# Optimization experiments

Measured on AMD Instinct MI355X. Metric: run time of the kernel, lower is better.

Reference implementation:

```python
import jax, jax.numpy as jnp
import numpy as np

EMBED = 512
HEADS = 8
DH = EMBED // HEADS  # 64
M = 256              # num_landmarks
ITERS = 6            # pinv iterations
SCALE = DH ** -0.5
RES_K = 33           # lucidrains residual_conv_kernel default


def _layer_norm(x, g, b, eps=1e-5):
    mu = jnp.mean(x, axis=-1, keepdims=True)
    var = jnp.mean((x - mu) ** 2, axis=-1, keepdims=True)
    return (x - mu) / jnp.sqrt(var + eps) * g + b


def _pinv_iter(x, iters=ITERS):
    # Moore-Penrose iterative pseudo-inverse (lucidrains nystrom-attention)
    abs_x = jnp.abs(x)
    denom = jnp.max(abs_x.sum(-1)) * jnp.max(abs_x.sum(-2))
    z = jnp.swapaxes(x, -1, -2) / denom
    I = jnp.eye(x.shape[-1], dtype=x.dtype)
    for _ in range(iters):
        xz = x @ z
        z = 0.25 * z @ (13 * I - xz @ (15 * I - xz @ (7 * I - xz)))
    return z


def _dwconv2d(x, w, b):
    # x: [B,C,H,W], w: [C,1,kh,kw] depthwise, SAME padding (odd kernels == k//2)
    out = jax.lax.conv_general_dilated(x, w, (1, 1), 'SAME',
                                       dimension_numbers=('NCHW', 'OIHW', 'NCHW'),
                                       feature_group_count=x.shape[1])
    return out + b[None, :, None, None]


def _nystrom_attn(x, Wqkv, Wo, bo, res_w):
    # x: [B, n, EMBED]; pad at FRONT so n divisible by M (matches F.pad(..., padding, 0) semantics)
    b, n, _ = x.shape
    pad = (M - n % M) % M
    x = jnp.pad(x, ((0, 0), (pad, 0), (0, 0)))
    npad = n + pad
    qkv = x @ Wqkv.T                               # [b, npad, 3*EMBED]
    q, k, v = jnp.split(qkv, 3, axis=-1)
    to_heads = lambda t: t.reshape(b, npad, HEADS, DH).transpose(0, 2, 1, 3)  # bhnd
    q, k, v = to_heads(q), to_heads(k), to_heads(v)
    q = q * SCALE
    l = npad // M
    q_land = q.reshape(b, HEADS, M, l, DH).mean(3)  # [b,h,M,d]
    k_land = k.reshape(b, HEADS, M, l, DH).mean(3)
    s1 = jnp.einsum('bhnd,bhmd->bhnm', q, k_land)
    s2 = jnp.einsum('bhmd,bhld->bhml', q_land, k_land)
    s3 = jnp.einsum('bhmd,bhnd->bhmn', q_land, k)
    a1 = jax.nn.softmax(s1, -1)
    a2 = jax.nn.softmax(s2, -1)
    a3 = jax.nn.softmax(s3, -1)
    a2_inv = _pinv_iter(a2)
    out = a1 @ (a2_inv @ (a3 @ v))                 # [b,h,npad,d]
    # residual depthwise conv over v: channels=heads, spatial=(npad, DH), kernel (33,1)
    res = jax.lax.conv_general_dilated(v, res_w, (1, 1), 'SAME',
                                       dimension_numbers=('NCHW', 'OIHW', 'NCHW'),
                                       feature_group_count=HEADS)
    out = out + res
    out = out.transpose(0, 2, 1, 3).reshape(b, npad, EMBED)
    out = out @ Wo.T + bo
    return out[:, -n:]                             # drop front padding


def setup_inputs() -> dict:
    key = jax.random.key(0)
    ks = jax.random.split(key, 32)
    s = 0.02
    inp = {}
    inp['data'] = jax.random.normal(ks[0], (4, 4096, 1536), jnp.float32)
    inp['W1'] = jax.random.normal(ks[1], (EMBED, 1536), jnp.float32) * s
    inp['b1'] = jnp.zeros((EMBED,), jnp.float32)
    inp['cls_token'] = jax.random.normal(ks[2], (1, 1, EMBED), jnp.float32)
    for li, base in ((1, 3), (2, 9)):
        inp[f'ln{li}_g'] = jnp.ones((EMBED,), jnp.float32)
        inp[f'ln{li}_b'] = jnp.zeros((EMBED,), jnp.float32)
        inp[f'Wqkv{li}'] = jax.random.normal(ks[base], (3 * EMBED, EMBED), jnp.float32) * s
        inp[f'Wo{li}'] = jax.random.normal(ks[base + 1], (EMBED, EMBED), jnp.float32) * s
        inp[f'bo{li}'] = jnp.zeros((EMBED,), jnp.float32)
        inp[f'res{li}'] = jax.random.normal(ks[base + 2], (HEADS, 1, RES_K, 1), jnp.float32) * s
    inp['pw7'] = jax.random.normal(ks[15], (EMBED, 1, 7, 7), jnp.float32) * s
    inp['pb7'] = jnp.zeros((EMBED,), jnp.float32)
    inp['pw5'] = jax.random.normal(ks[16], (EMBED, 1, 5, 5), jnp.float32) * s
    inp['pb5'] = jnp.zeros((EMBED,), jnp.float32)
    inp['pw3'] = jax.random.normal(ks[17], (EMBED, 1, 3, 3), jnp.float32) * s
    inp['pb3'] = jnp.zeros((EMBED,), jnp.float32)
    inp['lnf_g'] = jnp.ones((EMBED,), jnp.float32)
    inp['lnf_b'] = jnp.zeros((EMBED,), jnp.float32)
    inp['W2'] = jax.random.normal(ks[18], (2, EMBED), jnp.float32) * s
    inp['b2'] = jnp.zeros((2,), jnp.float32)
    return inp


def reference(data, W1, b1, cls_token, ln1_g, ln1_b, Wqkv1, Wo1, bo1, res1,
              ln2_g, ln2_b, Wqkv2, Wo2, bo2, res2,
              pw7, pb7, pw5, pb5, pw3, pb3, lnf_g, lnf_b, W2, b2):
    h = jax.nn.relu(data @ W1.T + b1)              # [B, N, EMBED]
    B, N, C = h.shape
    grid = int(np.ceil(np.sqrt(N)))
    add = grid * grid - N
    if add > 0:
        h = jnp.concatenate([h, h[:, :add]], axis=1)
    cls = jnp.broadcast_to(cls_token, (B, 1, C))
    h = jnp.concatenate([cls, h], axis=1)          # [B, 1+grid^2, C]
    # TransLayer 1
    h = h + _nystrom_attn(_layer_norm(h, ln1_g, ln1_b), Wqkv1, Wo1, bo1, res1)
    # PPEG
    cls_t, feat = h[:, :1], h[:, 1:]
    cnn = feat.transpose(0, 2, 1).reshape(B, C, grid, grid)
    x = _dwconv2d(cnn, pw7, pb7) + cnn + _dwconv2d(cnn, pw5, pb5) + _dwconv2d(cnn, pw3, pb3)
    feat = x.reshape(B, C, grid * grid).transpose(0, 2, 1)
    h = jnp.concatenate([cls_t, feat], axis=1)
    # TransLayer 2
    h = h + _nystrom_attn(_layer_norm(h, ln2_g, ln2_b), Wqkv2, Wo2, bo2, res2)
    h = _layer_norm(h, lnf_g, lnf_b)
    cls_feat = h[:, 0]
    logits = cls_feat @ W2.T + b2
    Y_prob = jax.nn.softmax(logits, -1)
    Y_hat = jnp.argmax(Y_prob, -1)
    return logits, Y_prob, Y_hat
```

## Files before the change

kernel.cpp:

```cpp
#include <hip/hip_runtime.h>
#include <math.h>

#define EMBED 512
#define HEADS 8
#define DH 64
#define MM 256
#define LSEG 17
#define NPAD 4352
#define NTOK 4097
#define N0 4096
#define BATCH 4
#define CIN 1536
#define QSCALE 0.125f
#define BH 32
#define NSEG 17

typedef float fp32x4 __attribute__((ext_vector_type(4)));
typedef short bf16x8 __attribute__((ext_vector_type(8)));
typedef short bf16x4 __attribute__((ext_vector_type(4)));
typedef unsigned short u16;

__device__ __forceinline__ unsigned short f2bf(float f) {
  unsigned int u = __float_as_uint(f);
  u += 0x7fffu + ((u >> 16) & 1u);
  return (unsigned short)(u >> 16);
}
__device__ __forceinline__ float bf2f(unsigned short u) {
  return __uint_as_float((unsigned)u << 16);
}

__device__ __forceinline__ float block_sum(float v, float* red) {
  #pragma unroll
  for (int o = 1; o < 64; o <<= 1) v += __shfl_xor(v, o);
  int lane = threadIdx.x & 63, wid = threadIdx.x >> 6;
  if (lane == 0) red[wid] = v;
  __syncthreads();
  float r = red[0] + red[1] + red[2] + red[3];
  __syncthreads();
  return r;
}
__device__ __forceinline__ float block_max(float v, float* red) {
  #pragma unroll
  for (int o = 1; o < 64; o <<= 1) v = fmaxf(v, __shfl_xor(v, o));
  int lane = threadIdx.x & 63, wid = threadIdx.x >> 6;
  if (lane == 0) red[wid] = v;
  __syncthreads();
  float r = fmaxf(fmaxf(red[0], red[1]), fmaxf(red[2], red[3]));
  __syncthreads();
  return r;
}

__global__ void f2bf_kernel(const float* __restrict__ in, u16* __restrict__ out, int n) {
  int t = (blockIdx.x * 256 + threadIdx.x) * 8;
  if (t >= n) return;
  float4 a = *(const float4*)&in[t];
  float4 b = *(const float4*)&in[t + 4];
  bf16x8 pk;
  pk[0]=(short)f2bf(a.x); pk[1]=(short)f2bf(a.y); pk[2]=(short)f2bf(a.z); pk[3]=(short)f2bf(a.w);
  pk[4]=(short)f2bf(b.x); pk[5]=(short)f2bf(b.y); pk[6]=(short)f2bf(b.z); pk[7]=(short)f2bf(b.w);
  *(bf16x8*)&out[t] = pk;
}

__global__ __launch_bounds__(256) void gemm_abt(
    const u16* __restrict__ A, const u16* __restrict__ W,
    int Mrows, int Ncols, int K, const float* __restrict__ bias,
    float* __restrict__ fout, float* __restrict__ fout2,
    u16* __restrict__ uo0, u16* __restrict__ uo1, u16* __restrict__ uo2,
    int mode)
{
  __shared__ u16 As[64][40];
  __shared__ u16 Ws[128][40];
  int tid = threadIdx.x;
  int lane = tid & 63;
  int wv = tid >> 6;
  int rowBase = blockIdx.y * 64, colBase = blockIdx.x * 128;
  int quad = lane >> 4;
  int l15 = lane & 15;
  int sr = tid >> 2;
  int skc = (tid & 3) * 8;

  fp32x4 acc[8];
  #pragma unroll
  for (int i = 0; i < 8; i++) acc[i] = fp32x4{0,0,0,0};

  for (int kb = 0; kb < K; kb += 32) {
    __syncthreads();
    {
      int grow = rowBase + sr;
      bf16x8 av;
      if (grow < Mrows) av = *(const bf16x8*)&A[(size_t)grow * K + kb + skc];
      else { bf16x8 z = {0,0,0,0,0,0,0,0}; av = z; }
      *(bf16x8*)&As[sr][skc] = av;
    }
    #pragma unroll
    for (int h = 0; h < 2; h++) {
      int r = sr + h * 64;
      *(bf16x8*)&Ws[r][skc] =
          *(const bf16x8*)&W[(size_t)(colBase + r) * K + kb + skc];
    }
    __syncthreads();
    bf16x8 aF = *(const bf16x8*)&As[wv * 16 + l15][quad * 8];
    #pragma unroll
    for (int ct = 0; ct < 8; ct++) {
      bf16x8 bF = *(const bf16x8*)&Ws[ct * 16 + l15][quad * 8];
      acc[ct] = __builtin_amdgcn_mfma_f32_16x16x32_bf16(aF, bF, acc[ct], 0, 0, 0);
    }
  }

  #pragma unroll
  for (int ct = 0; ct < 8; ct++) {
    int col = colBase + ct * 16 + l15;
    #pragma unroll
    for (int i = 0; i < 4; i++) {
      int row = rowBase + wv * 16 + quad * 4 + i;
      if (row >= Mrows) continue;
      float v = acc[ct][i];
      if (mode == 0) {
        v += bias[col];
        v = fmaxf(v, 0.f);
        int b = row / N0, n = row % N0;
        fout[((size_t)b * NTOK + 1 + n) * EMBED + col] = v;
      } else if (mode == 1) {
        int b = row / NPAD, n = row % NPAD;
        int sec = col / EMBED;
        int hh = (col % EMBED) / DH;
        int d = col & 63;
        u16* dst = (sec == 0) ? uo0 : ((sec == 1) ? uo1 : uo2);
        if (sec == 0) v *= QSCALE;
        dst[(((size_t)b * HEADS + hh) * NPAD + n) * DH + d] = f2bf(v);
      } else if (mode == 2) {
        v += bias[col];
        fout[(size_t)row * EMBED + col] += v;
      } else {
        v += bias[col];
        float full = fout[(size_t)row * EMBED + col] + v;
        fout[(size_t)row * EMBED + col] = full;
        int b = row / NTOK, t = row % NTOK;
        if (t > 0) fout2[((size_t)b * N0 + (t - 1)) * EMBED + col] = full;
      }
    }
  }
}

__global__ __launch_bounds__(256) void gemm_nn2(
    const u16* __restrict__ A, const u16* __restrict__ Bc,
    u16* __restrict__ Cr, u16* __restrict__ Cc,
    int Nsize, float beta, float sgn, float gamma)
{
  __shared__ u16 As[64][40];
  __shared__ u16 Bs[64][40];
  int batch = blockIdx.z;
  const u16* Ab = A + (size_t)batch * MM * MM;
  const u16* Bb = Bc + (size_t)batch * MM * Nsize;
  int tid = threadIdx.x;
  int lane = tid & 63, wv = tid >> 6, quad = lane >> 4, l15 = lane & 15;
  int rowBase = blockIdx.y * 64, colBase = blockIdx.x * 64;
  int sr = tid >> 2, skc = (tid & 3) * 8;
  fp32x4 acc[4] = {fp32x4{0,0,0,0}, fp32x4{0,0,0,0}, fp32x4{0,0,0,0}, fp32x4{0,0,0,0}};

  for (int kb = 0; kb < MM; kb += 32) {
    __syncthreads();
    *(bf16x8*)&As[sr][skc] = *(const bf16x8*)&Ab[(size_t)(rowBase + sr) * MM + kb + skc];
    *(bf16x8*)&Bs[sr][skc] = *(const bf16x8*)&Bb[(size_t)(colBase + sr) * MM + kb + skc];
    __syncthreads();
    bf16x8 aF = *(const bf16x8*)&As[wv * 16 + l15][quad * 8];
    #pragma unroll
    for (int ct = 0; ct < 4; ct++) {
      bf16x8 bF = *(const bf16x8*)&Bs[ct * 16 + l15][quad * 8];
      acc[ct] = __builtin_amdgcn_mfma_f32_16x16x32_bf16(aF, bF, acc[ct], 0, 0, 0);
    }
  }

  #pragma unroll
  for (int ct = 0; ct < 4; ct++) {
    int col = colBase + ct * 16 + l15;
    #pragma unroll
    for (int i = 0; i < 4; i++) {
      int row = rowBase + wv * 16 + quad * 4 + i;
      float v = sgn * acc[ct][i];
      if (beta != 0.f) v += beta * bf2f(Ab[(size_t)row * MM + col]);
      v *= gamma;
      u16 o = f2bf(v);
      if (Cr) Cr[(size_t)batch * MM * Nsize + (size_t)row * Nsize + col] = o;
      if (Cc) Cc[(size_t)batch * MM * Nsize + (size_t)col * MM + row] = o;
    }
  }
}

__global__ void cls_kernel(const float* __restrict__ cls, float* __restrict__ h) {
  int t = blockIdx.x * blockDim.x + threadIdx.x;
  if (t >= BATCH * EMBED) return;
  int b = t / EMBED, c = t % EMBED;
  h[(size_t)b * NTOK * EMBED + c] = cls[c];
}

__global__ void zero_pad_kernel(u16* __restrict__ xpad) {
  int t = blockIdx.x * blockDim.x + threadIdx.x;
  const int per = 255 * EMBED;
  if (t >= BATCH * per) return;
  int b = t / per, r = t % per;
  xpad[(size_t)b * NPAD * EMBED + r] = 0;
}

__global__ __launch_bounds__(256) void ln_pad_kernel(
    const float* __restrict__ h, const float* __restrict__ g,
    const float* __restrict__ be, u16* __restrict__ xpad)
{
  __shared__ float red[4];
  int row = blockIdx.x;
  int b = row / NTOK, j = row % NTOK;
  const float* x = h + (size_t)row * EMBED;
  int tid = threadIdx.x;
  float v0 = x[tid], v1 = x[tid + 256];
  float mu = block_sum(v0 + v1, red) * (1.f / 512.f);
  float d0 = v0 - mu, d1 = v1 - mu;
  float var = block_sum(d0 * d0 + d1 * d1, red) * (1.f / 512.f);
  float inv = 1.f / sqrtf(var + 1e-5f);
  u16* o = xpad + ((size_t)b * NPAD + 255 + j) * EMBED;
  o[tid]       = f2bf(d0 * inv * g[tid]       + be[tid]);
  o[tid + 256] = f2bf(d1 * inv * g[tid + 256] + be[tid + 256]);
}

__global__ __launch_bounds__(256) void landmarks_kernel(
    const u16* __restrict__ q, const u16* __restrict__ k,
    float* __restrict__ qland, float* __restrict__ kland, u16* __restrict__ klandB)
{
  int bh = blockIdx.y;
  int m = blockIdx.x * 4 + (threadIdx.x >> 6);
  int d = threadIdx.x & 63;
  const u16* qb = q + (size_t)bh * NPAD * DH;
  const u16* kb = k + (size_t)bh * NPAD * DH;
  float sq = 0.f, sk = 0.f;
  int base = m * LSEG;
  #pragma unroll
  for (int t = 0; t < LSEG; t++) {
    sq += bf2f(qb[(size_t)(base + t) * DH + d]);
    sk += bf2f(kb[(size_t)(base + t) * DH + d]);
  }
  float kv = sk * (1.f / LSEG);
  qland[((size_t)bh * MM + m) * DH + d] = sq * (1.f / LSEG);
  kland[((size_t)bh * MM + m) * DH + d] = kv;
  klandB[((size_t)bh * MM + m) * DH + d] = f2bf(kv);
}

__global__ __launch_bounds__(256) void s2_softmax_kernel(
    const float* __restrict__ qland, const float* __restrict__ kland,
    u16* __restrict__ a2)
{
  __shared__ float qrow[64];
  __shared__ float red[4];
  int bh = blockIdx.y, m = blockIdx.x, tid = threadIdx.x;
  if (tid < 64) qrow[tid] = qland[((size_t)bh * MM + m) * DH + tid];
  __syncthreads();
  const float* kb = kland + (size_t)bh * MM * DH + (size_t)tid * DH;
  float s = 0.f;
  #pragma unroll 16
  for (int d = 0; d < 64; d++) s += qrow[d] * kb[d];
  float mx = block_max(s, red);
  float e = __expf(s - mx);
  float tot = block_sum(e, red);
  a2[((size_t)bh * MM + m) * MM + tid] = f2bf(e / tot);
}

__global__ void init_denom_kernel(float* __restrict__ denoms) {
  if (threadIdx.x < 2) denoms[threadIdx.x] = 0.f;
}

__global__ __launch_bounds__(256) void denom_kernel(
    const u16* __restrict__ a2, float* __restrict__ denoms)
{
  __shared__ float red[4];
  int bh = blockIdx.x, tid = threadIdx.x;
  const u16* A = a2 + (size_t)bh * MM * MM;
  float rs = 0.f, cs = 0.f;
  for (int j = 0; j < MM; j++) rs += bf2f(A[(size_t)tid * MM + j]);
  for (int i = 0; i < MM; i++) cs += bf2f(A[(size_t)i * MM + tid]);
  float mr = block_max(rs, red);
  float mc = block_max(cs, red);
  if (tid == 0) {
    atomicMax((int*)&denoms[0], __float_as_int(mr));
    atomicMax((int*)&denoms[1], __float_as_int(mc));
  }
}

__global__ __launch_bounds__(256) void z0_trans_kernel(
    const u16* __restrict__ a2, const float* __restrict__ denoms,
    u16* __restrict__ zr, u16* __restrict__ zc)
{
  __shared__ u16 tile[64][72];
  int bh = blockIdx.z, i0 = blockIdx.y * 64, j0 = blockIdx.x * 64;
  int tid = threadIdx.x;
  float inv = 1.f / (denoms[0] * denoms[1]);
  const u16* Ab = a2 + (size_t)bh * MM * MM;
  #pragma unroll
  for (int it = 0; it < 4; it++) {
    int idx = it * 1024 + tid * 4;
    int r = idx >> 6, c = idx & 63;
    bf16x4 v = *(const bf16x4*)&Ab[(size_t)(i0 + r) * MM + j0 + c];
    u16 o[4];
    #pragma unroll
    for (int j = 0; j < 4; j++) o[j] = f2bf(bf2f((unsigned short)v[j]) * inv);
    *(bf16x4*)&zc[(size_t)bh * MM * MM + (size_t)(i0 + r) * MM + j0 + c] = *(bf16x4*)o;
    #pragma unroll
    for (int j = 0; j < 4; j++) tile[c + j][r] = o[j];
  }
  __syncthreads();
  #pragma unroll
  for (int it = 0; it < 4; it++) {
    int idx = it * 1024 + tid * 4;
    int r = idx >> 6, c = idx & 63;
    u16 o[4] = {tile[r][c], tile[r][c + 1], tile[r][c + 2], tile[r][c + 3]};
    *(bf16x4*)&zr[(size_t)bh * MM * MM + (size_t)(j0 + r) * MM + i0 + c] = *(bf16x4*)o;
  }
}

__global__ __launch_bounds__(256) void a3v_part_mfma(
    const float* __restrict__ qland, const u16* __restrict__ k,
    const u16* __restrict__ v, u16* __restrict__ Opart,
    float* __restrict__ mpart, float* __restrict__ lpart)
{
  __shared__ __align__(16) u16 qs[64][40];
  __shared__ __align__(16) u16 ks[256][72];
  __shared__ __align__(16) u16 vt[64][72];
  int tid = threadIdx.x;
  int lane = tid & 63, wv = tid >> 6, quad = lane >> 4, l15 = lane & 15;
  int bh = blockIdx.y;
  int ltile = blockIdx.x & 3;
  int seg = blockIdx.x >> 2;
  int l0 = ltile * 64;
  int key0 = seg * 256;
  const float* qb = qland + (size_t)bh * MM * DH;
  const u16* kb = k + (size_t)bh * NPAD * DH;
  const u16* vb = v + (size_t)bh * NPAD * DH;

  {
    int sr = tid >> 2, dc = (tid & 3) * 16;
    const float4* p = (const float4*)&qb[(size_t)(l0 + sr) * DH + dc];
    float4 v0 = p[0], v1 = p[1], v2 = p[2], v3 = p[3];
    float va[16] = {v0.x,v0.y,v0.z,v0.w, v1.x,v1.y,v1.z,v1.w,
                    v2.x,v2.y,v2.z,v2.w, v3.x,v3.y,v3.z,v3.w};
    bf16x8 p0, p1;
    #pragma unroll
    for (int j = 0; j < 8; j++) { p0[j] = (short)f2bf(va[j]); p1[j] = (short)f2bf(va[8 + j]); }
    *(bf16x8*)&qs[sr][dc] = p0;
    *(bf16x8*)&qs[sr][dc + 8] = p1;
  }
  #pragma unroll
  for (int i = 0; i < 16; i++) {
    int idx = i * 1024 + tid * 4;
    int r = idx >> 6, c = idx & 63;
    *(bf16x4*)&ks[r][c] = *(const bf16x4*)&kb[(size_t)(key0 + r) * DH + c];
  }
  __syncthreads();

  fp32x4 sacc[16];
  #pragma unroll
  for (int ct = 0; ct < 16; ct++) sacc[ct] = fp32x4{0,0,0,0};
  bf16x8 aF0 = *(const bf16x8*)&qs[wv * 16 + l15][quad * 8];
  bf16x8 aF1 = *(const bf16x8*)&qs[wv * 16 + l15][32 + quad * 8];
  #pragma unroll
  for (int ct = 0; ct < 16; ct++) {
    bf16x8 b0 = *(const bf16x8*)&ks[ct * 16 + l15][quad * 8];
    bf16x8 b1 = *(const bf16x8*)&ks[ct * 16 + l15][32 + quad * 8];
    sacc[ct] = __builtin_amdgcn_mfma_f32_16x16x32_bf16(aF0, b0, sacc[ct], 0, 0, 0);
    sacc[ct] = __builtin_amdgcn_mfma_f32_16x16x32_bf16(aF1, b1, sacc[ct], 0, 0, 0);
  }

  float mrow[4], lrow[4];
  #pragma unroll
  for (int i = 0; i < 4; i++) {
    float m = -3.0e38f;
    #pragma unroll
    for (int ct = 0; ct < 16; ct++) m = fmaxf(m, sacc[ct][i]);
    #pragma unroll
    for (int o = 1; o < 16; o <<= 1) m = fmaxf(m, __shfl_xor(m, o));
    float s = 0.f;
    #pragma unroll
    for (int ct = 0; ct < 16; ct++) {
      float e = __expf(sacc[ct][i] - m);
      sacc[ct][i] = e;
      s += e;
    }
    #pragma unroll
    for (int o = 1; o < 16; o <<= 1) s += __shfl_xor(s, o);
    mrow[i] = m;
    lrow[i] = s;
  }
  __syncthreads();
  u16* P = &ks[0][0];
  #pragma unroll
  for (int ct = 0; ct < 16; ct++)
    #pragma unroll
    for (int i = 0; i < 4; i++)
      P[(size_t)(wv * 16 + quad * 4 + i) * 264 + ct * 16 + l15] = f2bf(sacc[ct][i]);
  __syncthreads();

  fp32x4 oacc[4] = {fp32x4{0,0,0,0}, fp32x4{0,0,0,0}, fp32x4{0,0,0,0}, fp32x4{0,0,0,0}};
  int dh = tid & 63, kgrp = tid >> 6;
  for (int ch = 0; ch < 4; ch++) {
    if (ch) __syncthreads();
    {
      int kbase = kgrp * 16;
      #pragma unroll
      for (int g = 0; g < 4; g++) {
        u16 pk[4];
        #pragma unroll
        for (int r = 0; r < 4; r++)
          pk[r] = vb[(size_t)(key0 + ch * 64 + kbase + g * 4 + r) * DH + dh];
        *(bf16x4*)&vt[dh][kbase + g * 4] = *(bf16x4*)pk;
      }
    }
    __syncthreads();
    #pragma unroll
    for (int ks2 = 0; ks2 < 2; ks2++) {
      bf16x8 aP = *(const bf16x8*)&P[(size_t)(wv * 16 + l15) * 264 + ch * 64 + ks2 * 32 + quad * 8];
      #pragma unroll
      for (int ct = 0; ct < 4; ct++) {
        bf16x8 bV = *(const bf16x8*)&vt[ct * 16 + l15][ks2 * 32 + quad * 8];
        oacc[ct] = __builtin_amdgcn_mfma_f32_16x16x32_bf16(aP, bV, oacc[ct], 0, 0, 0);
      }
    }
  }

  size_t base = ((size_t)seg * BH + bh) * MM + l0;
  #pragma unroll
  for (int ct = 0; ct < 4; ct++)
    #pragma unroll
    for (int i = 0; i < 4; i++) {
      int row = wv * 16 + quad * 4 + i;
      Opart[(base + row) * DH + ct * 16 + l15] = f2bf(oacc[ct][i]);
    }
  if (l15 == 0) {
    #pragma unroll
    for (int i = 0; i < 4; i++) {
      int row = wv * 16 + quad * 4 + i;
      mpart[base + row] = mrow[i];
      lpart[base + row] = lrow[i];
    }
  }
}

__global__ __launch_bounds__(256) void a3v_merge_kernel(
    const u16* __restrict__ Opart, const float* __restrict__ mpart,
    const float* __restrict__ lpart, u16* __restrict__ kvT)
{
  int bh = blockIdx.y;
  int lbase = blockIdx.x * 64;
  int d = threadIdx.x & 63, lsub = threadIdx.x >> 6;
  for (int li = lsub; li < 64; li += 4) {
    int lm = lbase + li;
    float M = -3.0e38f;
    #pragma unroll
    for (int s = 0; s < NSEG; s++)
      M = fmaxf(M, mpart[((size_t)s * BH + bh) * MM + lm]);
    float L = 0.f, O = 0.f;
    #pragma unroll
    for (int s = 0; s < NSEG; s++) {
      size_t idx = ((size_t)s * BH + bh) * MM + lm;
      float w = __expf(mpart[idx] - M);
      L += lpart[idx] * w;
      O += bf2f(Opart[idx * DH + d]) * w;
    }
    kvT[((size_t)bh * DH + d) * MM + lm] = f2bf(O / L);
  }
}

__global__ void prep_toep_kernel(const float* __restrict__ resw0,
                                 const float* __restrict__ resw1,
                                 u16* __restrict__ toepB)
{
  int i = blockIdx.x * 256 + threadIdx.x;
  if (i >= 2 * 8 * 64 * 96) return;
  int t = i % 96, r = (i / 96) % 64, hh = (i / (96 * 64)) % 8, l = i / (96 * 64 * 8);
  const float* rw = l ? resw1 : resw0;
  int tap = t - r;
  float v = (tap >= 0 && tap <= 32) ? rw[hh * 33 + tap] : 0.f;
  toepB[i] = f2bf(v);
}

__global__ __launch_bounds__(256, 4) void attn1_mfma(
    const u16* __restrict__ q, const u16* __restrict__ klandB,
    const u16* __restrict__ kv2T, const u16* __restrict__ v,
    const u16* __restrict__ toep, u16* __restrict__ attn)
{
  __shared__ __align__(16) u16 buf[64 * 264];
  int tid = threadIdx.x;
  int lane = tid & 63, wv = tid >> 6, quad = lane >> 4, l15 = lane & 15;
  int bh = blockIdx.y, b = bh >> 3, hh = bh & 7;
  int n0 = 255 + blockIdx.x * 64;
  const u16* qb  = q + (size_t)bh * NPAD * DH;
  const u16* klb = klandB + (size_t)bh * MM * DH;
  const u16* kvb = kv2T + (size_t)bh * DH * MM;
  const u16* vb  = v + (size_t)bh * NPAD * DH;
  const u16* tb  = toep + (size_t)hh * 64 * 96;

  int qrow = n0 + wv * 16 + l15; if (qrow > NPAD - 1) qrow = NPAD - 1;
  bf16x8 aF0 = *(const bf16x8*)&qb[(size_t)qrow * DH + quad * 8];
  bf16x8 aF1 = *(const bf16x8*)&qb[(size_t)qrow * DH + 32 + quad * 8];
  fp32x4 sacc[16];
  #pragma unroll
  for (int ct = 0; ct < 16; ct++) sacc[ct] = fp32x4{0,0,0,0};
  #pragma unroll
  for (int ct = 0; ct < 16; ct++) {
    bf16x8 b0 = *(const bf16x8*)&klb[(size_t)(ct * 16 + l15) * DH + quad * 8];
    bf16x8 b1 = *(const bf16x8*)&klb[(size_t)(ct * 16 + l15) * DH + 32 + quad * 8];
    sacc[ct] = __builtin_amdgcn_mfma_f32_16x16x32_bf16(aF0, b0, sacc[ct], 0, 0, 0);
    sacc[ct] = __builtin_amdgcn_mfma_f32_16x16x32_bf16(aF1, b1, sacc[ct], 0, 0, 0);
  }
  #pragma unroll
  for (int i = 0; i < 4; i++) {
    float m = -3.0e38f;
    #pragma unroll
    for (int ct = 0; ct < 16; ct++) m = fmaxf(m, sacc[ct][i]);
    #pragma unroll
    for (int o = 1; o < 16; o <<= 1) m = fmaxf(m, __shfl_xor(m, o));
    float s = 0.f;
    #pragma unroll
    for (int ct = 0; ct < 16; ct++) {
      float e = __expf(sacc[ct][i] - m);
      sacc[ct][i] = e;
      s += e;
    }
    #pragma unroll
    for (int o = 1; o < 16; o <<= 1) s += __shfl_xor(s, o);
    float inv = 1.f / s;
    #pragma unroll
    for (int ct = 0; ct < 16; ct++) sacc[ct][i] *= inv;
  }
  #pragma unroll
  for (int ct = 0; ct < 16; ct++)
    #pragma unroll
    for (int i = 0; i < 4; i++)
      buf[(size_t)(wv * 16 + quad * 4 + i) * 264 + ct * 16 + l15] = f2bf(sacc[ct][i]);
  __syncthreads();

  fp32x4 oacc[4] = {fp32x4{0,0,0,0}, fp32x4{0,0,0,0}, fp32x4{0,0,0,0}, fp32x4{0,0,0,0}};
  #pragma unroll
  for (int ks = 0; ks < 8; ks++) {
    bf16x8 aP = *(const bf16x8*)&buf[(size_t)(wv * 16 + l15) * 264 + ks * 32 + quad * 8];
    #pragma unroll
    for (int ct = 0; ct < 4; ct++) {
      bf16x8 bV = *(const bf16x8*)&kvb[(size_t)(ct * 16 + l15) * MM + ks * 32 + quad * 8];
      oacc[ct] = __builtin_amdgcn_mfma_f32_16x16x32_bf16(aP, bV, oacc[ct], 0, 0, 0);
    }
  }
  __syncthreads();

  {
    int d = lane;
    #pragma unroll
    for (int tt4 = 0; tt4 < 6; tt4++) {
      u16 vals[4];
      #pragma unroll
      for (int j = 0; j < 4; j++) {
        int t = wv * 24 + tt4 * 4 + j;
        int g = n0 - 16 + t;
        vals[j] = (g <= NPAD - 1) ? vb[(size_t)g * DH + d] : (u16)0;
      }
      *(bf16x4*)&buf[d * 104 + wv * 24 + tt4 * 4] = *(bf16x4*)vals;
    }
  }
  __syncthreads();

  #pragma unroll
  for (int kc = 0; kc < 3; kc++) {
    bf16x8 aT = *(const bf16x8*)&tb[(size_t)(wv * 16 + l15) * 96 + kc * 32 + quad * 8];
    #pragma unroll
    for (int ct = 0; ct < 4; ct++) {
      bf16x8 bW = *(const bf16x8*)&buf[(ct * 16 + l15) * 104 + kc * 32 + quad * 8];
      oacc[ct] = __builtin_amdgcn_mfma_f32_16x16x32_bf16(aT, bW, oacc[ct], 0, 0, 0);
    }
  }

  #pragma unroll
  for (int ct = 0; ct < 4; ct++) {
    int c = ct * 16 + l15;
    #pragma unroll
    for (int i = 0; i < 4; i++) {
      int rl = wv * 16 + quad * 4 + i;
      int n = n0 + rl;
      if (n > NPAD - 1) continue;
      attn[((size_t)b * NTOK + (n - 255)) * EMBED + hh * DH + c] = f2bf(oacc[ct][i]);
    }
  }
}

__global__ void prep_wcomb_kernel(
    const float* __restrict__ pw7, const float* __restrict__ pw5,
    const float* __restrict__ pw3, const float* __restrict__ pb7,
    const float* __restrict__ pb5, const float* __restrict__ pb3,
    float* __restrict__ wcomb, float* __restrict__ biasc)
{
  int i = blockIdx.x * blockDim.x + threadIdx.x;
  if (i < EMBED * 49) {
    int c = i / 49, tap = i % 49;
    int ky = tap / 7, kx = tap % 7;
    float v = pw7[c * 49 + tap];
    if (ky >= 1 && ky <= 5 && kx >= 1 && kx <= 5) v += pw5[c * 25 + (ky - 1) * 5 + (kx - 1)];
    if (ky >= 2 && ky <= 4 && kx >= 2 && kx <= 4) v += pw3[c * 9 + (ky - 2) * 3 + (kx - 2)];
    if (ky == 3 && kx == 3) v += 1.f;
    wcomb[tap * EMBED + c] = v;
  }
  if (i < EMBED) biasc[i] = pb7[i] + pb5[i] + pb3[i];
}

__global__ __launch_bounds__(256) void dwconv_kernel(
    const float* __restrict__ tmp, const float* __restrict__ wcomb,
    const float* __restrict__ biasc, float* __restrict__ h)
{
  __shared__ float4 wsm[49][32];
  int tx = threadIdx.x;
  int ty = threadIdx.y;
  int cb = blockIdx.x * 128;
  int c = cb + tx * 4;
  int b = blockIdx.z;
  int n = blockIdx.y * 8 + ty;
  int y = n >> 6, x = n & 63;
  int tid = ty * 32 + tx;
  for (int i = tid; i < 49 * 32; i += 256) {
    int tap = i >> 5, g = i & 31;
    wsm[tap][g] = *(const float4*)&wcomb[tap * EMBED + cb + g * 4];
  }
  __syncthreads();
  const float* src = tmp + (size_t)b * N0 * EMBED;
  float4 acc = *(const float4*)&biasc[c];
  #pragma unroll
  for (int ky = 0; ky < 7; ky++) {
    int yy = y + ky - 3;
    if (yy < 0 || yy >= 64) continue;
    #pragma unroll
    for (int kx = 0; kx < 7; kx++) {
      int xx = x + kx - 3;
      if (xx < 0 || xx >= 64) continue;
      float4 vv = *(const float4*)&src[((size_t)yy * 64 + xx) * EMBED + c];
      float4 w = wsm[ky * 7 + kx][tx];
      acc.x += vv.x * w.x;
      acc.y += vv.y * w.y;
      acc.z += vv.z * w.z;
      acc.w += vv.w * w.w;
    }
  }
  *(float4*)&h[((size_t)b * NTOK + 1 + n) * EMBED + c] = acc;
}

__global__ __launch_bounds__(256) void final_kernel(
    const float* __restrict__ h, const float* __restrict__ g,
    const float* __restrict__ be, const float* __restrict__ W2,
    const float* __restrict__ b2, float* __restrict__ out)
{
  __shared__ float red[4];
  int b = blockIdx.x, tid = threadIdx.x;
  const float* x = h + (size_t)b * NTOK * EMBED;
  float v0 = x[tid], v1 = x[tid + 256];
  float mu = block_sum(v0 + v1, red) * (1.f / 512.f);
  float d0 = v0 - mu, d1 = v1 - mu;
  float var = block_sum(d0 * d0 + d1 * d1, red) * (1.f / 512.f);
  float inv = 1.f / sqrtf(var + 1e-5f);
  float xn0 = d0 * inv * g[tid] + be[tid];
  float xn1 = d1 * inv * g[tid + 256] + be[tid + 256];
  float l0 = block_sum(xn0 * W2[tid] + xn1 * W2[tid + 256], red);
  float l1 = block_sum(xn0 * W2[512 + tid] + xn1 * W2[512 + tid + 256], red);
  if (tid == 0) {
    l0 += b2[0]; l1 += b2[1];
    out[b * 2 + 0] = l0;
    out[b * 2 + 1] = l1;
    float mx = fmaxf(l0, l1);
    float e0 = expf(l0 - mx), e1 = expf(l1 - mx);
    float s = e0 + e1;
    out[8 + b * 2 + 0] = e0 / s;
    out[8 + b * 2 + 1] = e1 / s;
    out[16 + b] = (l1 > l0) ? 1.f : 0.f;
  }
}

extern "C" void kernel_launch(void* const* d_in, const int* in_sizes, int n_in,
                              void* d_out, int out_size, void* d_ws, size_t ws_size,
                              hipStream_t stream)
{
  const float* data = (const float*)d_in[0];
  const float* W1   = (const float*)d_in[1];
  const float* b1   = (const float*)d_in[2];
  const float* cls  = (const float*)d_in[3];
  const float* lng[2]  = {(const float*)d_in[4],  (const float*)d_in[10]};
  const float* lnb[2]  = {(const float*)d_in[5],  (const float*)d_in[11]};
  const float* Wqkv[2] = {(const float*)d_in[6],  (const float*)d_in[12]};
  const float* Wo[2]   = {(const float*)d_in[7],  (const float*)d_in[13]};
  const float* bo[2]   = {(const float*)d_in[8],  (const float*)d_in[14]};
  const float* resw[2] = {(const float*)d_in[9],  (const float*)d_in[15]};
  const float* pw7 = (const float*)d_in[16];
  const float* pb7 = (const float*)d_in[17];
  const float* pw5 = (const float*)d_in[18];
  const float* pb5 = (const float*)d_in[19];
  const float* pw3 = (const float*)d_in[20];
  const float* pb3 = (const float*)d_in[21];
  const float* lnfg = (const float*)d_in[22];
  const float* lnfb = (const float*)d_in[23];
  const float* W2  = (const float*)d_in[24];
  const float* b2  = (const float*)d_in[25];

  float* ws = (float*)d_ws;
  size_t off = 0;
  auto alloc = [&](size_t n) { float* p = ws + off; off += n; return p; };
  float* hbuf   = alloc((size_t)BATCH * NTOK * EMBED);
  float* xpadf  = alloc((size_t)BATCH * NPAD * EMBED);
  float* qbuff  = alloc((size_t)BH * NPAD * DH);
  float* kbuff  = alloc((size_t)BH * NPAD * DH);
  float* vbuff  = alloc((size_t)BH * NPAD * DH);
  float* qland  = alloc((size_t)BH * MM * DH);
  float* kland  = alloc((size_t)BH * MM * DH);
  float* klandBf= alloc((size_t)BH * MM * DH / 2);
  float* a2f    = alloc((size_t)BH * MM * MM / 2);
  float* zaRf   = alloc((size_t)BH * MM * MM / 2);
  float* zaCf   = alloc((size_t)BH * MM * MM / 2);
  float* zbRf   = alloc((size_t)BH * MM * MM / 2);
  float* zbCf   = alloc((size_t)BH * MM * MM / 2);
  float* xzRf   = alloc((size_t)BH * MM * MM / 2);
  float* xzCf   = alloc((size_t)BH * MM * MM / 2);
  float* t1Cf   = alloc((size_t)BH * MM * MM / 2);
  float* t2Cf   = alloc((size_t)BH * MM * MM / 2);
  float* kvTf   = alloc((size_t)BH * MM * DH / 2);
  float* kv2Tf  = alloc((size_t)BH * MM * DH / 2);
  float* wqkvbf = alloc((size_t)2 * 3 * EMBED * EMBED / 2);
  float* wobf   = alloc((size_t)2 * EMBED * EMBED / 2);
  float* toepf  = alloc((size_t)2 * 8 * 64 * 96 / 2);
  float* wcomb  = alloc(49 * EMBED);
  float* biasc  = alloc(EMBED);
  float* denoms = alloc(64);
  float* mpart  = alloc((size_t)NSEG * BH * MM);
  float* lpart  = alloc((size_t)NSEG * BH * MM);

  u16* xpadB = (u16*)xpadf;
  u16* qB = (u16*)qbuff;
  u16* kB = (u16*)kbuff;
  u16* vB = (u16*)vbuff;
  u16* klandB = (u16*)klandBf;
  u16* a2B = (u16*)a2f;
  u16* zaR = (u16*)zaRf; u16* zaC = (u16*)zaCf;
  u16* zbR = (u16*)zbRf; u16* zbC = (u16*)zbCf;
  u16* xzR = (u16*)xzRf; u16* xzC = (u16*)xzCf;
  u16* t1C = (u16*)t1Cf; u16* t2C = (u16*)t2Cf;
  u16* kvT = (u16*)kvTf; u16* kv2T = (u16*)kv2Tf;
  u16* attnB = xpadB;
  u16* OpartB = zaR;
  u16* databf = (u16*)qbuff;
  u16* W1bf = (u16*)vbuff;
  u16* WqkvB[2] = {(u16*)wqkvbf, (u16*)wqkvbf + (size_t)3 * EMBED * EMBED};
  u16* WoB[2]   = {(u16*)wobf,   (u16*)wobf + (size_t)EMBED * EMBED};
  u16* toepB[2] = {(u16*)toepf,  (u16*)toepf + (size_t)8 * 64 * 96};
  float* convtmp = qbuff;

  int ndata = BATCH * N0 * CIN;
  f2bf_kernel<<<dim3((ndata / 8 + 255) / 256), 256, 0, stream>>>(data, databf, ndata);
  f2bf_kernel<<<dim3((EMBED * CIN / 8 + 255) / 256), 256, 0, stream>>>(W1, W1bf, EMBED * CIN);
  for (int l = 0; l < 2; l++) {
    f2bf_kernel<<<dim3((3 * EMBED * EMBED / 8 + 255) / 256), 256, 0, stream>>>(Wqkv[l], WqkvB[l], 3 * EMBED * EMBED);
    f2bf_kernel<<<dim3((EMBED * EMBED / 8 + 255) / 256), 256, 0, stream>>>(Wo[l], WoB[l], EMBED * EMBED);
  }
  prep_toep_kernel<<<dim3((2 * 8 * 64 * 96 + 255) / 256), 256, 0, stream>>>(
      resw[0], resw[1], (u16*)toepf);

  gemm_abt<<<dim3(EMBED / 128, (BATCH * N0) / 64), 256, 0, stream>>>(
      databf, W1bf, BATCH * N0, EMBED, CIN, b1, hbuf, nullptr, nullptr, nullptr, nullptr, 0);
  cls_kernel<<<dim3((BATCH * EMBED + 255) / 256), 256, 0, stream>>>(cls, hbuf);

  for (int layer = 0; layer < 2; layer++) {
    ln_pad_kernel<<<dim3(BATCH * NTOK), 256, 0, stream>>>(hbuf, lng[layer], lnb[layer], xpadB);
    zero_pad_kernel<<<dim3((BATCH * 255 * EMBED + 255) / 256), 256, 0, stream>>>(xpadB);
    gemm_abt<<<dim3((3 * EMBED) / 128, (BATCH * NPAD) / 64), 256, 0, stream>>>(
        xpadB, WqkvB[layer], BATCH * NPAD, 3 * EMBED, EMBED, nullptr,
        nullptr, nullptr, qB, kB, vB, 1);
    landmarks_kernel<<<dim3(MM / 4, BH), 256, 0, stream>>>(qB, kB, qland, kland, klandB);
    s2_softmax_kernel<<<dim3(MM, BH), 256, 0, stream>>>(qland, kland, a2B);
    init_denom_kernel<<<1, 64, 0, stream>>>(denoms);
    denom_kernel<<<dim3(BH), 256, 0, stream>>>(a2B, denoms);

    a3v_part_mfma<<<dim3(4 * NSEG, BH), 256, 0, stream>>>(
        qland, kB, vB, OpartB, mpart, lpart);
    a3v_merge_kernel<<<dim3(MM / 64, BH), 256, 0, stream>>>(OpartB, mpart, lpart, kvT);

    z0_trans_kernel<<<dim3(4, 4, BH), 256, 0, stream>>>(a2B, denoms, zaR, zaC);
    u16 *zinR = zaR, *zinC = zaC, *zoutR = zbR, *zoutC = zbC;
    for (int it = 0; it < 6; it++) {
      gemm_nn2<<<dim3(4, 4, BH), 256, 0, stream>>>(a2B, zinC, xzR, xzC, MM, 0.f, 1.f, 1.f);
      gemm_nn2<<<dim3(4, 4, BH), 256, 0, stream>>>(xzR, xzC, nullptr, t1C, MM, 7.f, -1.f, 1.f);
      gemm_nn2<<<dim3(4, 4, BH), 256, 0, stream>>>(xzR, t1C, nullptr, t2C, MM, 15.f, -1.f, 1.f);
      gemm_nn2<<<dim3(4, 4, BH), 256, 0, stream>>>(zinR, t2C, zoutR, zoutC, MM, 13.f, -1.f, 0.25f);
      u16* t;
      t = zinR; zinR = zoutR; zoutR = t;
      t = zinC; zinC = zoutC; zoutC = t;
    }
    gemm_nn2<<<dim3(1, 4, BH), 256, 0, stream>>>(zinR, kvT, nullptr, kv2T, DH, 0.f, 1.f, 1.f);
    attn1_mfma<<<dim3((NTOK + 63) / 64, BH), 256, 0, stream>>>(
        qB, klandB, kv2T, vB, toepB[layer], attnB);
    gemm_abt<<<dim3(EMBED / 128, (BATCH * NTOK + 63) / 64), 256, 0, stream>>>(
        attnB, WoB[layer], BATCH * NTOK, EMBED, EMBED, bo[layer], hbuf,
        (layer == 0) ? convtmp : nullptr, nullptr, nullptr, nullptr,
        (layer == 0) ? 3 : 2);

    if (layer == 0) {
      prep_wcomb_kernel<<<dim3((EMBED * 49 + 255) / 256), 256, 0, stream>>>(
          pw7, pw5, pw3, pb7, pb5, pb3, wcomb, biasc);
      dwconv_kernel<<<dim3(EMBED / 128, N0 / 8, BATCH), dim3(32, 8), 0, stream>>>(
          convtmp, wcomb, biasc, hbuf);
    }
  }

  final_kernel<<<dim3(BATCH), 256, 0, stream>>>(hbuf, lnfg, lnfb, W2, b2, (float*)d_out);
}
```

Baseline: 1.617 ms.

## Restructure pinv iteration into three GEMM stages and batch loads in attention kernel

The Newton-Schulz pseudo-inverse step is expanded algebraically as 0.25·(zY)(7Y−Y²) − 3.75·zY + 3.25·z. The two independent products, Y·(7I−Y) and z·Y, run in one merged launch, which cuts each iteration from four dependent GEMM launches to three. Separately, attn1_mfma now preloads groups of B-fragments into registers before issuing MFMAs, and its launch bounds drop from 4 to 2 blocks per CU. That trades occupancy for more in-flight loads. The reordered polynomial changes where bf16 rounding happens, so numerics shift slightly.

Measured after the change: 1.589 ms. No clear change (-1.7%).

```diff
diff --git a/kernel.cpp b/kernel.cpp
--- a/kernel.cpp
+++ b/kernel.cpp
@@ -142,10 +142,11 @@
   }
 }
 
-__global__ __launch_bounds__(256) void gemm_nn2(
+__global__ __launch_bounds__(256) void pinv_gemm(
     const u16* __restrict__ A, const u16* __restrict__ Bc,
+    const u16* __restrict__ E,
     u16* __restrict__ Cr, u16* __restrict__ Cc,
-    int Nsize, float beta, float sgn, float gamma)
+    int Nsize, float gamma, float beta, float eps)
 {
   __shared__ u16 As[64][40];
   __shared__ u16 Bs[64][40];
@@ -177,12 +178,57 @@
     #pragma unroll
     for (int i = 0; i < 4; i++) {
       int row = rowBase + wv * 16 + quad * 4 + i;
-      float v = sgn * acc[ct][i];
+      float v = gamma * acc[ct][i];
       if (beta != 0.f) v += beta * bf2f(Ab[(size_t)row * MM + col]);
-      v *= gamma;
+      if (eps != 0.f)  v += eps * bf2f(E[(size_t)batch * MM * MM + (size_t)row * MM + col]);
       u16 o = f2bf(v);
       if (Cr) Cr[(size_t)batch * MM * Nsize + (size_t)row * Nsize + col] = o;
       if (Cc) Cc[(size_t)batch * MM * Nsize + (size_t)col * MM + row] = o;
+    }
+  }
+}
+
+__global__ __launch_bounds__(256) void pinv_um(
+    const u16* __restrict__ YR, const u16* __restrict__ YC,
+    const u16* __restrict__ zR, u16* __restrict__ UC, u16* __restrict__ MR)
+{
+  __shared__ u16 As[64][40];
+  __shared__ u16 Bs[64][40];
+  int which = blockIdx.z >> 5;
+  int batch = blockIdx.z & 31;
+  const u16* Ab = (which ? zR : YR) + (size_t)batch * MM * MM;
+  const u16* Bb = YC + (size_t)batch * MM * MM;
+  int tid = threadIdx.x;
+  int lane = tid & 63, wv = tid >> 6, quad = lane >> 4, l15 = lane & 15;
+  int rowBase = blockIdx.y * 64, colBase = blockIdx.x * 64;
+  int sr = tid >> 2, skc = (tid & 3) * 8;
+  fp32x4 acc[4] = {fp32x4{0,0,0,0}, fp32x4{0,0,0,0}, fp32x4{0,0,0,0}, fp32x4{0,0,0,0}};
+
+  for (int kb = 0; kb < MM; kb += 32) {
+    __syncthreads();
+    *(bf16x8*)&As[sr][skc] = *(const bf16x8*)&Ab[(size_t)(rowBase + sr) * MM + kb + skc];
+    *(bf16x8*)&Bs[sr][skc] = *(const bf16x8*)&Bb[(size_t)(colBase + sr) * MM + kb + skc];
+    __syncthreads();
+    bf16x8 aF = *(const bf16x8*)&As[wv * 16 + l15][quad * 8];
+    #pragma unroll
+    for (int ct = 0; ct < 4; ct++) {
+      bf16x8 bF = *(const bf16x8*)&Bs[ct * 16 + l15][quad * 8];
+      acc[ct] = __builtin_amdgcn_mfma_f32_16x16x32_bf16(aF, bF, acc[ct], 0, 0, 0);
+    }
+  }
+
+  #pragma unroll
+  for (int ct = 0; ct < 4; ct++) {
+    int col = colBase + ct * 16 + l15;
+    #pragma unroll
+    for (int i = 0; i < 4; i++) {
+      int row = rowBase + wv * 16 + quad * 4 + i;
+      if (which == 0) {
+        float v = 7.f * bf2f(Ab[(size_t)row * MM + col]) - acc[ct][i];
+        UC[(size_t)batch * MM * MM + (size_t)col * MM + row] = f2bf(v);
+      } else {
+        MR[(size_t)batch * MM * MM + (size_t)row * MM + col] = f2bf(acc[ct][i]);
+      }
     }
   }
 }
@@ -478,7 +524,7 @@
   toepB[i] = f2bf(v);
 }
 
-__global__ __launch_bounds__(256, 4) void attn1_mfma(
+__global__ __launch_bounds__(256, 2) void attn1_mfma(
     const u16* __restrict__ q, const u16* __restrict__ klandB,
     const u16* __restrict__ kv2T, const u16* __restrict__ v,
     const u16* __restrict__ toep, u16* __restrict__ attn)
@@ -501,11 +547,20 @@
   #pragma unroll
   for (int ct = 0; ct < 16; ct++) sacc[ct] = fp32x4{0,0,0,0};
   #pragma unroll
-  for (int ct = 0; ct < 16; ct++) {
-    bf16x8 b0 = *(const bf16x8*)&klb[(size_t)(ct * 16 + l15) * DH + quad * 8];
-    bf16x8 b1 = *(const bf16x8*)&klb[(size_t)(ct * 16 + l15) * DH + 32 + quad * 8];
-    sacc[ct] = __builtin_amdgcn_mfma_f32_16x16x32_bf16(aF0, b0, sacc[ct], 0, 0, 0);
-    sacc[ct] = __builtin_amdgcn_mfma_f32_16x16x32_bf16(aF1, b1, sacc[ct], 0, 0, 0);
+  for (int g = 0; g < 2; g++) {
+    bf16x8 b0[8], b1[8];
+    #pragma unroll
+    for (int j = 0; j < 8; j++) {
+      int ct = g * 8 + j;
+      b0[j] = *(const bf16x8*)&klb[(size_t)(ct * 16 + l15) * DH + quad * 8];
+      b1[j] = *(const bf16x8*)&klb[(size_t)(ct * 16 + l15) * DH + 32 + quad * 8];
+    }
+    #pragma unroll
+    for (int j = 0; j < 8; j++) {
+      int ct = g * 8 + j;
+      sacc[ct] = __builtin_amdgcn_mfma_f32_16x16x32_bf16(aF0, b0[j], sacc[ct], 0, 0, 0);
+      sacc[ct] = __builtin_amdgcn_mfma_f32_16x16x32_bf16(aF1, b1[j], sacc[ct], 0, 0, 0);
+    }
   }
   #pragma unroll
   for (int i = 0; i < 4; i++) {
@@ -536,13 +591,21 @@
 
   fp32x4 oacc[4] = {fp32x4{0,0,0,0}, fp32x4{0,0,0,0}, fp32x4{0,0,0,0}, fp32x4{0,0,0,0}};
   #pragma unroll
-  for (int ks = 0; ks < 8; ks++) {
-    bf16x8 aP = *(const bf16x8*)&buf[(size_t)(wv * 16 + l15) * 264 + ks * 32 + quad * 8];
-    #pragma unroll
-    for (int ct = 0; ct < 4; ct++) {
-      bf16x8 bV = *(const bf16x8*)&kvb[(size_t)(ct * 16 + l15) * MM + ks * 32 + quad * 8];
-      oacc[ct] = __builtin_amdgcn_mfma_f32_16x16x32_bf16(aP, bV, oacc[ct], 0, 0, 0);
-    }
+  for (int g = 0; g < 2; g++) {
+    bf16x8 ap[4], bv[4][4];
+    #pragma unroll
+    for (int j = 0; j < 4; j++) {
+      int ks = g * 4 + j;
+      ap[j] = *(const bf16x8*)&buf[(size_t)(wv * 16 + l15) * 264 + ks * 32 + quad * 8];
+      #pragma unroll
+      for (int ct = 0; ct < 4; ct++)
+        bv[j][ct] = *(const bf16x8*)&kvb[(size_t)(ct * 16 + l15) * MM + ks * 32 + quad * 8];
+    }
+    #pragma unroll
+    for (int j = 0; j < 4; j++)
+      #pragma unroll
+      for (int ct = 0; ct < 4; ct++)
+        oacc[ct] = __builtin_amdgcn_mfma_f32_16x16x32_bf16(ap[j], bv[j][ct], oacc[ct], 0, 0, 0);
   }
   __syncthreads();
 
@@ -562,13 +625,18 @@
   }
   __syncthreads();
 
-  #pragma unroll
-  for (int kc = 0; kc < 3; kc++) {
-    bf16x8 aT = *(const bf16x8*)&tb[(size_t)(wv * 16 + l15) * 96 + kc * 32 + quad * 8];
-    #pragma unroll
-    for (int ct = 0; ct < 4; ct++) {
-      bf16x8 bW = *(const bf16x8*)&buf[(ct * 16 + l15) * 104 + kc * 32 + quad * 8];
-      oacc[ct] = __builtin_amdgcn_mfma_f32_16x16x32_bf16(aT, bW, oacc[ct], 0, 0, 0);
+  {
+    bf16x8 at[3];
+    #pragma unroll
+    for (int kc = 0; kc < 3; kc++)
+      at[kc] = *(const bf16x8*)&tb[(size_t)(wv * 16 + l15) * 96 + kc * 32 + quad * 8];
+    #pragma unroll
+    for (int kc = 0; kc < 3; kc++) {
+      #pragma unroll
+      for (int ct = 0; ct < 4; ct++) {
+        bf16x8 bW = *(const bf16x8*)&buf[(ct * 16 + l15) * 104 + kc * 32 + quad * 8];
+        oacc[ct] = __builtin_amdgcn_mfma_f32_16x16x32_bf16(at[kc], bW, oacc[ct], 0, 0, 0);
+      }
     }
   }
 
@@ -714,10 +782,10 @@
   float* zaCf   = alloc((size_t)BH * MM * MM / 2);
   float* zbRf   = alloc((size_t)BH * MM * MM / 2);
   float* zbCf   = alloc((size_t)BH * MM * MM / 2);
-  float* xzRf   = alloc((size_t)BH * MM * MM / 2);
-  float* xzCf   = alloc((size_t)BH * MM * MM / 2);
-  float* t1Cf   = alloc((size_t)BH * MM * MM / 2);
-  float* t2Cf   = alloc((size_t)BH * MM * MM / 2);
+  float* YRf    = alloc((size_t)BH * MM * MM / 2);
+  float* YCf    = alloc((size_t)BH * MM * MM / 2);
+  float* UCf    = alloc((size_t)BH * MM * MM / 2);
+  float* MRf    = alloc((size_t)BH * MM * MM / 2);
   float* kvTf   = alloc((size_t)BH * MM * DH / 2);
   float* kv2Tf  = alloc((size_t)BH * MM * DH / 2);
   float* wqkvbf = alloc((size_t)2 * 3 * EMBED * EMBED / 2);
@@ -737,8 +805,8 @@
   u16* a2B = (u16*)a2f;
   u16* zaR = (u16*)zaRf; u16* zaC = (u16*)zaCf;
   u16* zbR = (u16*)zbRf; u16* zbC = (u16*)zbCf;
-  u16* xzR = (u16*)xzRf; u16* xzC = (u16*)xzCf;
-  u16* t1C = (u16*)t1Cf; u16* t2C = (u16*)t2Cf;
+  u16* YR = (u16*)YRf; u16* YC = (u16*)YCf;
+  u16* UC = (u16*)UCf; u16* MR = (u16*)MRf;
   u16* kvT = (u16*)kvTf; u16* kv2T = (u16*)kv2Tf;
   u16* attnB = xpadB;
   u16* OpartB = zaR;
@@ -781,15 +849,17 @@
     z0_trans_kernel<<<dim3(4, 4, BH), 256, 0, stream>>>(a2B, denoms, zaR, zaC);
     u16 *zinR = zaR, *zinC = zaC, *zoutR = zbR, *zoutC = zbC;
     for (int it = 0; it < 6; it++) {
-      gemm_nn2<<<dim3(4, 4, BH), 256, 0, stream>>>(a2B, zinC, xzR, xzC, MM, 0.f, 1.f, 1.f);
-      gemm_nn2<<<dim3(4, 4, BH), 256, 0, stream>>>(xzR, xzC, nullptr, t1C, MM, 7.f, -1.f, 1.f);
-      gemm_nn2<<<dim3(4, 4, BH), 256, 0, stream>>>(xzR, t1C, nullptr, t2C, MM, 15.f, -1.f, 1.f);
-      gemm_nn2<<<dim3(4, 4, BH), 256, 0, stream>>>(zinR, t2C, zoutR, zoutC, MM, 13.f, -1.f, 0.25f);
+      pinv_gemm<<<dim3(4, 4, BH), 256, 0, stream>>>(
+          a2B, zinC, nullptr, YR, YC, MM, 1.f, 0.f, 0.f);
+      pinv_um<<<dim3(4, 4, 2 * BH), 256, 0, stream>>>(YR, YC, zinR, UC, MR);
+      pinv_gemm<<<dim3(4, 4, BH), 256, 0, stream>>>(
+          MR, UC, zinR, zoutR, zoutC, MM, 0.25f, -3.75f, 3.25f);
       u16* t;
       t = zinR; zinR = zoutR; zoutR = t;
       t = zinC; zinC = zoutC; zoutC = t;
     }
-    gemm_nn2<<<dim3(1, 4, BH), 256, 0, stream>>>(zinR, kvT, nullptr, kv2T, DH, 0.f, 1.f, 1.f);
+    pinv_gemm<<<dim3(1, 4, BH), 256, 0, stream>>>(
+        zinR, kvT, nullptr, nullptr, kv2T, DH, 1.f, 0.f, 0.f);
     attn1_mfma<<<dim3((NTOK + 63) / 64, BH), 256, 0, stream>>>(
         qB, klandB, kv2T, vB, toepB[layer], attnB);
     gemm_abt<<<dim3(EMBED / 128, (BATCH * NTOK + 63) / 64), 256, 0, stream>>>(
```
